# Kernel tuning notes

Hardware: AMD Instinct MI355X
Metric: run time of the kernel (lower is better)

The kernel has to match this reference:

```python
import jax, jax.numpy as jnp
import numpy as np

N = 32768   # total nodes
B = 128     # graphs
S = 256     # nodes per graph (equal-size graphs)
E = 524288  # edges
DIN = 128   # in_dim
DH = 256    # hidden_dim
H = 8       # heads
DFF = 1024  # ffn hidden
EPS = 1e-5


def _seg_sum(x, idx, num):
    return jax.ops.segment_sum(x, idx, num_segments=num)


def _bn(x, g, b):
    # BatchNorm1d with batch statistics (training-mode math, deterministic)
    mu = jnp.mean(x, axis=0)
    var = jnp.mean((x - mu) ** 2, axis=0)
    return (x - mu) * jax.lax.rsqrt(var + EPS) * g + b


def _ln(x, g, b):
    mu = jnp.mean(x, axis=-1, keepdims=True)
    var = jnp.mean((x - mu) ** 2, axis=-1, keepdims=True)
    return (x - mu) * jax.lax.rsqrt(var + EPS) * g + b


def _gcn_conv(x, W, bias, edge_index, n):
    # PyG GCNConv: h = x W; add self-loops; norm = d^-1/2[row] * d^-1/2[col]; scatter-add at col
    h = x @ W
    loop = jnp.arange(n)
    row = jnp.concatenate([edge_index[0], loop])
    col = jnp.concatenate([edge_index[1], loop])
    deg = _seg_sum(jnp.ones_like(col, dtype=h.dtype), col, n)  # >=1 due to self-loops
    dis = jax.lax.rsqrt(jnp.maximum(deg, 1.0))
    norm = dis[row] * dis[col]
    out = _seg_sum(h[row] * norm[:, None], col, n)
    return out + bias


def setup_inputs() -> dict:
    key = jax.random.key(0)
    ks = jax.random.split(key, 24)

    def w(i, shape, scale=0.05):
        return jax.random.normal(ks[i], shape, dtype=jnp.float32) * scale

    return {
        "x": jax.random.normal(ks[0], (N, DIN), dtype=jnp.float32),
        "edge_index": jax.random.randint(ks[1], (2, E), 0, N, dtype=jnp.int32),
        "batch": jnp.repeat(jnp.arange(B, dtype=jnp.int32), S),
        "inter_f": jax.random.normal(ks[2], (B, DH), dtype=jnp.float32),
        "bn1_g": jnp.ones((DIN,), jnp.float32), "bn1_b": jnp.zeros((DIN,), jnp.float32),
        "bn2_g": jnp.ones((DH,), jnp.float32), "bn2_b": jnp.zeros((DH,), jnp.float32),
        "w_conv1": w(3, (DIN, DH)), "b_conv1": jnp.zeros((DH,), jnp.float32),
        "w_conv2": w(4, (DH, DH)), "b_conv2": jnp.zeros((DH,), jnp.float32),
        "wq": w(5, (DH, DH)), "bq": jnp.zeros((DH,), jnp.float32),
        "wk": w(6, (DH, DH)), "bk": jnp.zeros((DH,), jnp.float32),
        "wv": w(7, (DH, DH)), "bv": jnp.zeros((DH,), jnp.float32),
        "wo": w(8, (DH, DH)), "bo": jnp.zeros((DH,), jnp.float32),
        "ln1_g": jnp.ones((DH,), jnp.float32), "ln1_b": jnp.zeros((DH,), jnp.float32),
        "ln2_g": jnp.ones((DH,), jnp.float32), "ln2_b": jnp.zeros((DH,), jnp.float32),
        "w_ff1": w(9, (DH, DFF)), "b_ff1": jnp.zeros((DFF,), jnp.float32),
        "w_ff2": w(10, (DFF, DH)), "b_ff2": jnp.zeros((DH,), jnp.float32),
    }


def reference(x, edge_index, batch, inter_f,
              bn1_g, bn1_b, bn2_g, bn2_b,
              w_conv1, b_conv1, w_conv2, b_conv2,
              wq, bq, wk, bk, wv, bv, wo, bo,
              ln1_g, ln1_b, ln2_g, ln2_b,
              w_ff1, b_ff1, w_ff2, b_ff2):
    n = x.shape[0]
    hd = DH // H
    # init_avg_h: scatter-mean of raw x per graph
    cnt = _seg_sum(jnp.ones((n,), x.dtype), batch, B)
    init_avg_h = _seg_sum(x, batch, B) / jnp.maximum(cnt, 1.0)[:, None]
    # layer 1 (dropout = identity in eval)
    h = _bn(x, bn1_g, bn1_b)
    h = jax.nn.relu(_gcn_conv(h, w_conv1, b_conv1, edge_index, n))
    # layer 2 with residual
    pre = h
    h2 = _bn(h, bn2_g, bn2_b)
    h = pre + jax.nn.relu(_gcn_conv(h2, w_conv2, b_conv2, edge_index, n))
    # transformer block: inject per-graph feature, self-attend within each graph
    inter_h = inter_f[batch]
    t = (h + inter_h).reshape(B, S, DH)
    q = (t @ wq + bq).reshape(B, S, H, hd)
    k = (t @ wk + bk).reshape(B, S, H, hd)
    v = (t @ wv + bv).reshape(B, S, H, hd)
    scores = jnp.einsum('bqhd,bkhd->bhqk', q, k) / jnp.sqrt(jnp.float32(hd))
    attn = jax.nn.softmax(scores, axis=-1)
    o = jnp.einsum('bhqk,bkhd->bqhd', attn, v).reshape(B, S, DH) @ wo + bo
    t2 = _ln(t + o, ln1_g, ln1_b)
    ffn = jax.nn.relu(t2 @ w_ff1 + b_ff1) @ w_ff2 + b_ff2
    t3 = _ln(t2 + ffn, ln2_g, ln2_b)
    hg = t3.reshape(n, DH)
    readout = _seg_sum(hg, batch, B)
    return readout, init_avg_h
```

## Files before the change

kernel.cpp:

```cpp
#include <hip/hip_runtime.h>
#include <math.h>

#define NN   32768
#define BG   128
#define SG   256
#define EE   524288
#define DIN_ 128
#define DH_  256
#define NH   8
#define HD_  32
#define DFF_ 1024
#define EPS_ 1e-5f

typedef __attribute__((ext_vector_type(8))) short bf16x8;
typedef __attribute__((ext_vector_type(4))) float f32x4;
typedef __attribute__((ext_vector_type(2))) unsigned int u32x2;
typedef __attribute__((ext_vector_type(4))) unsigned int u32x4;

__device__ __forceinline__ unsigned short f2bf(float f) {
    unsigned int u = __builtin_bit_cast(unsigned int, f);
    unsigned int r = u + 0x7FFFu + ((u >> 16) & 1u);
    return (unsigned short)(r >> 16);
}
__device__ __forceinline__ float bf2f(unsigned short u) {
    return __builtin_bit_cast(float, (unsigned int)u << 16);
}
__device__ __forceinline__ void glds16(const unsigned short* g, unsigned short* l) {
    __builtin_amdgcn_global_load_lds(
        (const __attribute__((address_space(1))) void*)g,
        (__attribute__((address_space(3))) void*)l, 16, 0, 0);
}
#define WAIT_VM0() __builtin_amdgcn_s_waitcnt(0x0F70)
#define WAIT_VM1() __builtin_amdgcn_s_waitcnt(0x0F71)
#define WAIT_VM2() __builtin_amdgcn_s_waitcnt(0x0F72)
#define WAIT_VM3() __builtin_amdgcn_s_waitcnt(0x0F73)
#define WAIT_VM4() __builtin_amdgcn_s_waitcnt(0x0F74)

#define QSCALE (0.17677669529663689f * 1.4426950408889634f)

__global__ __launch_bounds__(128) void initstats_kernel(const float* __restrict__ X,
                                                        float* __restrict__ out2,
                                                        float* __restrict__ csum,
                                                        float* __restrict__ csumsq) {
    int b = blockIdx.x, j = threadIdx.x;
    float s = 0.f, sq = 0.f;
    for (int r = 0; r < SG; ++r) {
        float v = X[(size_t)(b * SG + r) * DIN_ + j];
        s += v; sq += v * v;
    }
    out2[b * DIN_ + j] = s * (1.f / (float)SG);
    atomicAdd(&csum[j], s);
    atomicAdd(&csumsq[j], sq);
}

template <int C>
__global__ __launch_bounds__(C) void bnfin_kernel(const float* __restrict__ csum,
                                                  const float* __restrict__ csumsq,
                                                  const float* __restrict__ g,
                                                  const float* __restrict__ b,
                                                  float* __restrict__ scale,
                                                  float* __restrict__ shift) {
    int j = threadIdx.x;
    float mu  = csum[j] * (1.f / (float)NN);
    float var = csumsq[j] * (1.f / (float)NN) - mu * mu;
    float s = g[j] * rsqrtf(var + EPS_);
    scale[j] = s;
    shift[j] = b[j] - mu * s;
}

template <int C>
__global__ __launch_bounds__(256) void bnapply_kernel(const float* __restrict__ X,
                                                      const float* __restrict__ sc,
                                                      const float* __restrict__ sh,
                                                      unsigned short* __restrict__ Y) {
    int i = blockIdx.x * 256 + threadIdx.x;
    int j = i & (C - 1);
    Y[i] = f2bf(X[i] * sc[j] + sh[j]);
}

__global__ __launch_bounds__(256) void wtrans_kernel(const float* __restrict__ W,
                                                     unsigned short* __restrict__ Wt,
                                                     int K, int N, float scale) {
    int idx = blockIdx.x * 256 + threadIdx.x;
    if (idx < K * N) {
        int n = idx / K, k = idx - n * K;
        Wt[idx] = f2bf(W[(size_t)k * N + n] * scale);
    }
}

__global__ __launch_bounds__(256) void bcat_kernel(const float* __restrict__ bq,
                                                   const float* __restrict__ bk,
                                                   const float* __restrict__ bv,
                                                   float* __restrict__ o) {
    int j = threadIdx.x;
    if (blockIdx.x == 0) o[j] = bq[j] * QSCALE;
    else if (blockIdx.x == 1) o[DH_ + j] = bk[j];
    else o[2 * DH_ + j] = bv[j];
}

__global__ __launch_bounds__(256) void deg_kernel(const int* __restrict__ col,
                                                  int* __restrict__ deg) {
    int e = blockIdx.x * 256 + threadIdx.x;
    if (e < EE) atomicAdd(&deg[col[e]], 1);
}

__global__ __launch_bounds__(1024) void scan_kernel(const int* __restrict__ deg,
                                                    int* __restrict__ off,
                                                    float* __restrict__ dis) {
    __shared__ int sums[1024];
    int t = threadIdx.x;
    int base = t * 32;
    int loc[32];
    int run = 0;
#pragma unroll
    for (int i = 0; i < 32; ++i) { loc[i] = run; run += deg[base + i]; }
    sums[t] = run;
    __syncthreads();
    for (int d = 1; d < 1024; d <<= 1) {
        int tmp = (t >= d) ? sums[t - d] : 0;
        __syncthreads();
        sums[t] += tmp;
        __syncthreads();
    }
    int excl = sums[t] - run;
#pragma unroll
    for (int i = 0; i < 32; ++i) {
        off[base + i] = excl + loc[i];
        dis[base + i] = rsqrtf((float)(deg[base + i] + 1));
    }
    if (t == 1023) off[NN] = sums[1023];
}

__global__ __launch_bounds__(256) void scatter_kernel(const int* __restrict__ row,
                                                      const int* __restrict__ col,
                                                      const int* __restrict__ off,
                                                      int* __restrict__ cnt,
                                                      int* __restrict__ srow) {
    int e = blockIdx.x * 256 + threadIdx.x;
    if (e < EE) {
        int c = col[e];
        int p = off[c] + atomicAdd(&cnt[c], 1);
        srow[p] = row[e];
    }
}

template <int C, int FUSE_BN>
__global__ __launch_bounds__(256) void aggb_kernel(const unsigned short* __restrict__ X,
                                                   const int* __restrict__ off,
                                                   const int* __restrict__ srow,
                                                   const float* __restrict__ dis,
                                                   const float* __restrict__ scl,
                                                   const float* __restrict__ shf,
                                                   unsigned short* __restrict__ Y) {
    constexpr int EPL = C / 64;
    int lane = threadIdx.x & 63;
    int c = blockIdx.x * 4 + (threadIdx.x >> 6);
    float dc = dis[c];
    float acc[EPL];
    float wsum = dc;
    {
        unsigned short t[EPL];
        const unsigned short* xc = X + (size_t)c * C + lane * EPL;
        if constexpr (EPL == 4) *(uint2*)t = *(const uint2*)xc;
        else *(unsigned int*)t = *(const unsigned int*)xc;
#pragma unroll
        for (int e2 = 0; e2 < EPL; ++e2) acc[e2] = dc * bf2f(t[e2]);
    }
    int s = off[c], en = off[c + 1];
    int i = s;
    for (; i + 4 <= en; i += 4) {
        int r0 = srow[i], r1 = srow[i + 1], r2 = srow[i + 2], r3 = srow[i + 3];
        float d0 = dis[r0], d1 = dis[r1], d2 = dis[r2], d3 = dis[r3];
        unsigned short t0[EPL], t1[EPL], t2[EPL], t3[EPL];
        const unsigned short* p0 = X + (size_t)r0 * C + lane * EPL;
        const unsigned short* p1 = X + (size_t)r1 * C + lane * EPL;
        const unsigned short* p2 = X + (size_t)r2 * C + lane * EPL;
        const unsigned short* p3 = X + (size_t)r3 * C + lane * EPL;
        if constexpr (EPL == 4) {
            *(uint2*)t0 = *(const uint2*)p0;
            *(uint2*)t1 = *(const uint2*)p1;
            *(uint2*)t2 = *(const uint2*)p2;
            *(uint2*)t3 = *(const uint2*)p3;
        } else {
            *(unsigned int*)t0 = *(const unsigned int*)p0;
            *(unsigned int*)t1 = *(const unsigned int*)p1;
            *(unsigned int*)t2 = *(const unsigned int*)p2;
            *(unsigned int*)t3 = *(const unsigned int*)p3;
        }
        wsum += d0 + d1 + d2 + d3;
#pragma unroll
        for (int e2 = 0; e2 < EPL; ++e2) {
            acc[e2] += d0 * bf2f(t0[e2]) + d1 * bf2f(t1[e2]) +
                       d2 * bf2f(t2[e2]) + d3 * bf2f(t3[e2]);
        }
    }
    for (; i < en; ++i) {
        int r = srow[i];
        float dr = dis[r];
        unsigned short t[EPL];
        const unsigned short* xr = X + (size_t)r * C + lane * EPL;
        if constexpr (EPL == 4) *(uint2*)t = *(const uint2*)xr;
        else *(unsigned int*)t = *(const unsigned int*)xr;
        wsum += dr;
#pragma unroll
        for (int e2 = 0; e2 < EPL; ++e2) acc[e2] += dr * bf2f(t[e2]);
    }
    unsigned short t[EPL];
#pragma unroll
    for (int e2 = 0; e2 < EPL; ++e2) {
        float v;
        if constexpr (FUSE_BN) {
            int j = lane * EPL + e2;
            v = dc * (scl[j] * acc[e2] + shf[j] * wsum);
        } else {
            v = dc * acc[e2];
        }
        t[e2] = f2bf(v);
    }
    unsigned short* yc = Y + (size_t)c * C + lane * EPL;
    if constexpr (EPL == 4) *(uint2*)yc = *(const uint2*)t;
    else *(unsigned int*)yc = *(const unsigned int*)t;
}

__global__ __launch_bounds__(512, 8) void gemm_bf16_kernel(
    const unsigned short* __restrict__ A,
    const unsigned short* __restrict__ Bt,
    unsigned short* __restrict__ Cb,
    int M, int K, int N,
    const float* __restrict__ bias,
    const unsigned short* __restrict__ resb,
    const float* __restrict__ inter,
    int do_relu, int relu_first) {
    constexpr int LDP = 32;
    constexpr int CP = 136;
    constexpr int MI = 2;
    constexpr int STG = 8192;
    constexpr int BOFS = 4096;
    __shared__ unsigned short Smem[3 * STG];
    unsigned short* Cs = Smem;
    int gx = gridDim.x, gyP = gridDim.y >> 3;
    int d = blockIdx.y * gx + blockIdx.x;
    int xcd = d & 7, j2 = d >> 3;
    int bm = (xcd * gyP + j2 / gx) * 128;
    int bn = (j2 % gx) * 128;
    int tid = threadIdx.x;
    int wave = tid >> 6, lane = tid & 63;
    int wm = (wave >> 1) * 32;
    int wn = (wave & 1) * 64;
    int lrc = lane & 15;
    int koct = lane >> 4;
    int rsw = (lrc >> 1) & 3;
    int rofs = (koct ^ rsw) * 8;
    int cg = (lane & 3) ^ ((lane >> 3) & 3);
    int skk = cg * 8;

    int sr = wave * 16 + (lane >> 2);
    const unsigned short* gA0 = A + (size_t)(bm + sr) * K + skk;
    const unsigned short* gB0 = Bt + (size_t)(bn + sr) * K + skk;
    int lofs = wave * 512 + lane * 8;

    f32x4 acc[MI][4];
#pragma unroll
    for (int i = 0; i < MI; ++i)
#pragma unroll
        for (int j = 0; j < 4; ++j) acc[i][j] = (f32x4){0.f, 0.f, 0.f, 0.f};

    glds16(gA0, Smem + lofs);
    glds16(gB0, Smem + BOFS + lofs);
    glds16(gA0 + 32, Smem + STG + lofs);
    glds16(gB0 + 32, Smem + STG + BOFS + lofs);

    int rb = 0;
    for (int k0 = 0; k0 < K; k0 += 32) {
        if (k0 + 64 < K) {
            int wb = rb + 2; if (wb >= 3) wb -= 3;
            unsigned short* ld = Smem + wb * STG;
            glds16(gA0 + k0 + 64, ld + lofs);
            glds16(gB0 + k0 + 64, ld + BOFS + lofs);
            WAIT_VM4();
        } else if (k0 + 32 < K) {
            WAIT_VM2();
        } else {
            WAIT_VM0();
        }
        __builtin_amdgcn_s_barrier();
        const unsigned short* Ab = Smem + rb * STG;
        const unsigned short* Bb = Ab + BOFS;
        bf16x8 af[MI], bfr[4];
#pragma unroll
        for (int i = 0; i < MI; ++i)
            af[i] = *(const bf16x8*)(Ab + (wm + i * 16 + lrc) * LDP + rofs);
#pragma unroll
        for (int j = 0; j < 4; ++j)
            bfr[j] = *(const bf16x8*)(Bb + (wn + j * 16 + lrc) * LDP + rofs);
#pragma unroll
        for (int i = 0; i < MI; ++i)
#pragma unroll
            for (int j = 0; j < 4; ++j)
                acc[i][j] = __builtin_amdgcn_mfma_f32_16x16x32_bf16(af[i], bfr[j],
                                                                    acc[i][j], 0, 0, 0);
        __builtin_amdgcn_s_barrier();
        rb = (rb + 1 == 3) ? 0 : rb + 1;
    }
#pragma unroll
    for (int i = 0; i < MI; ++i) {
#pragma unroll
        for (int r = 0; r < 4; ++r) {
            int lrow = wm + i * 16 + koct * 4 + r;
            int grow = bm + lrow;
#pragma unroll
            for (int j = 0; j < 4; ++j) {
                int lcol = wn + j * 16 + lrc;
                int gcol = bn + lcol;
                float v = acc[i][j][r];
                if (bias) v += bias[gcol];
                if (relu_first) v = fmaxf(v, 0.f);
                if (resb) v += bf2f(resb[(size_t)grow * N + gcol]);
                if (inter) v += inter[(grow >> 8) * N + gcol];
                if (do_relu && !relu_first) v = fmaxf(v, 0.f);
                Cs[lrow * CP + lcol] = f2bf(v);
            }
        }
    }
    __syncthreads();
#pragma unroll
    for (int it = 0; it < 4; ++it) {
        int row = it * 32 + (tid >> 4);
        int cc = (tid & 15) * 8;
        *(uint4*)(&Cb[(size_t)(bm + row) * N + bn + cc]) =
            *(const uint4*)(&Cs[row * CP + cc]);
    }
}

template <int MODE>
__global__ __launch_bounds__(512, 8) void gemm32n256_kernel(
    const unsigned short* __restrict__ A,
    const unsigned short* __restrict__ Bt,
    unsigned short* __restrict__ Cb,
    int K,
    const float* __restrict__ bias,
    const unsigned short* __restrict__ resb,
    const float* __restrict__ inter,
    int do_relu, int relu_first,
    float* __restrict__ stat0, float* __restrict__ stat1,
    const float* __restrict__ lng, const float* __restrict__ lnbt,
    float* __restrict__ outp) {
    constexpr int LDP = 32;
    constexpr int CP = 264;
    constexpr int STG = 9216;
    constexpr int BOFS = 1024;
    __shared__ unsigned short Smem[2 * STG];
    unsigned short* Cs = Smem;
    int bm = blockIdx.x * 32;
    int tid = threadIdx.x;
    int wave = tid >> 6, lane = tid & 63;
    int wm = (wave >> 2) * 16;
    int wn = (wave & 3) * 64;
    int lrc = lane & 15;
    int koct = lane >> 4;
    int rsw = (lrc >> 1) & 3;
    int rofs = (koct ^ rsw) * 8;
    int cg = (lane & 3) ^ ((lane >> 3) & 3);
    int skk = cg * 8;

    const unsigned short* gB0 = Bt + (size_t)(wave * 32 + (lane >> 2)) * K + skk;
    size_t g16 = (size_t)16 * K;
    int lofsB = BOFS + wave * 1024 + lane * 8;
    const unsigned short* gA0 = nullptr;
    int lofsA = 0;
    if (wave < 2) {
        gA0 = A + (size_t)(bm + wave * 16 + (lane >> 2)) * K + skk;
        lofsA = wave * 512 + lane * 8;
    }

    f32x4 acc[4];
#pragma unroll
    for (int j = 0; j < 4; ++j) acc[j] = (f32x4){0.f, 0.f, 0.f, 0.f};

    glds16(gB0, Smem + lofsB);
    glds16(gB0 + g16, Smem + lofsB + 512);
    if (wave < 2) glds16(gA0, Smem + lofsA);

    int cur = 0;
    for (int k0 = 0; k0 < K; k0 += 32) {
        int nk = k0 + 32;
        if (nk < K) {
            unsigned short* nb = Smem + (cur ^ 1) * STG;
            glds16(gB0 + nk, nb + lofsB);
            glds16(gB0 + nk + g16, nb + lofsB + 512);
            if (wave < 2) {
                glds16(gA0 + nk, nb + lofsA);
                WAIT_VM3();
            } else {
                WAIT_VM2();
            }
        } else {
            WAIT_VM0();
        }
        __builtin_amdgcn_s_barrier();
        const unsigned short* Ab = Smem + cur * STG;
        const unsigned short* Bb = Ab + BOFS;
        bf16x8 af = *(const bf16x8*)(Ab + (wm + lrc) * LDP + rofs);
        bf16x8 bfr[4];
#pragma unroll
        for (int j = 0; j < 4; ++j)
            bfr[j] = *(const bf16x8*)(Bb + (wn + j * 16 + lrc) * LDP + rofs);
#pragma unroll
        for (int j = 0; j < 4; ++j)
            acc[j] = __builtin_amdgcn_mfma_f32_16x16x32_bf16(af, bfr[j], acc[j], 0, 0, 0);
        __builtin_amdgcn_s_barrier();
        cur ^= 1;
    }
#pragma unroll
    for (int r = 0; r < 4; ++r) {
        int lrow = wm + koct * 4 + r;
        int grow = bm + lrow;
#pragma unroll
        for (int j = 0; j < 4; ++j) {
            int lcol = wn + j * 16 + lrc;
            float v = acc[j][r];
            if (bias) v += bias[lcol];
            if (relu_first) v = fmaxf(v, 0.f);
            if (resb) v += bf2f(resb[(size_t)grow * 256 + lcol]);
            if (inter) v += inter[(grow >> 8) * 256 + lcol];
            if (do_relu && !relu_first) v = fmaxf(v, 0.f);
            Cs[lrow * CP + lcol] = f2bf(v);
        }
    }
    __syncthreads();

    if constexpr (MODE == 0 || MODE == 1) {
#pragma unroll
        for (int it = 0; it < 2; ++it) {
            int row = it * 16 + (tid >> 5);
            int cc = (tid & 31) * 8;
            *(uint4*)(&Cb[(size_t)(bm + row) * 256 + cc]) =
                *(const uint4*)(&Cs[row * CP + cc]);
        }
        if constexpr (MODE == 1) {
            if (tid < 256) {
                float s = 0.f, sq = 0.f;
                for (int r = 0; r < 32; ++r) {
                    float v = bf2f(Cs[r * CP + tid]);
                    s += v; sq += v * v;
                }
                atomicAdd(&stat0[tid], s);
                atomicAdd(&stat1[tid], sq);
            }
        }
    } else {
        float4 g4 = *(const float4*)(lng + lane * 4);
        float4 b4 = *(const float4*)(lnbt + lane * 4);
#pragma unroll
        for (int q = 0; q < 4; ++q) {
            int row = wave * 4 + q;
            unsigned short tv[4];
            *(uint2*)tv = *(const uint2*)(Cs + row * CP + lane * 4);
            float v0 = bf2f(tv[0]), v1 = bf2f(tv[1]), v2 = bf2f(tv[2]), v3 = bf2f(tv[3]);
            float sum = v0 + v1 + v2 + v3;
#pragma unroll
            for (int off = 32; off; off >>= 1) sum += __shfl_xor(sum, off);
            float mu = sum * (1.f / (float)DH_);
            float d0 = v0 - mu, d1 = v1 - mu, d2 = v2 - mu, d3 = v3 - mu;
            float vs = d0 * d0 + d1 * d1 + d2 * d2 + d3 * d3;
#pragma unroll
            for (int off = 32; off; off >>= 1) vs += __shfl_xor(vs, off);
            float rs = rsqrtf(vs * (1.f / (float)DH_) + EPS_);
            unsigned short ov[4];
            ov[0] = f2bf(d0 * rs * g4.x + b4.x);
            ov[1] = f2bf(d1 * rs * g4.y + b4.y);
            ov[2] = f2bf(d2 * rs * g4.z + b4.z);
            ov[3] = f2bf(d3 * rs * g4.w + b4.w);
            if constexpr (MODE == 2) {
                *(uint2*)(&Cb[(size_t)(bm + row) * 256 + lane * 4]) = *(uint2*)ov;
            } else {
                *(uint2*)(Cs + row * CP + lane * 4) = *(uint2*)ov;
            }
        }
        if constexpr (MODE == 3) {
            __syncthreads();
            if (tid < 256) {
                float s = 0.f;
                for (int r = 0; r < 32; ++r) s += bf2f(Cs[r * CP + tid]);
                atomicAdd(&outp[(bm >> 8) * 256 + tid], s);
            }
        }
    }
}

__global__ __launch_bounds__(256, 4) void attn_mfma_kernel(
    const unsigned short* __restrict__ QKV,
    unsigned short* __restrict__ Ob) {
    int b = blockIdx.x >> 3, h = blockIdx.x & 7;
    __shared__ unsigned short Ks[256 * 32];
    __shared__ unsigned short Vt[32 * 264];
    __shared__ float Lc[4 * 64];
    const unsigned short* kg = QKV + (size_t)b * 256 * 768 + 256 + h * 32;
    const unsigned short* vg = QKV + (size_t)b * 256 * 768 + 512 + h * 32;
    int tid = threadIdx.x;
#pragma unroll
    for (int it = 0; it < 4; ++it) {
        int c = it * 256 + tid;
        int row = c >> 2, ch = c & 3;
        int slot = ch ^ ((row >> 1) & 3);
        *(uint4*)(Ks + row * 32 + slot * 8) =
            *(const uint4*)(kg + (size_t)row * 768 + ch * 8);
    }
#pragma unroll
    for (int it = 0; it < 4; ++it) {
        int c = it * 256 + tid;
        int key = c >> 2, d0 = (c & 3) * 8;
        unsigned short tmp[8];
        *(uint4*)tmp = *(const uint4*)(vg + (size_t)key * 768 + d0);
#pragma unroll
        for (int j = 0; j < 8; ++j) Vt[(d0 + j) * 264 + key] = tmp[j];
    }
    __syncthreads();

    int wave = tid >> 6, lane = tid & 63;
    int lr = lane & 15, koct = lane >> 4;
    int s4 = (lr >> 1) & 3;
    int qrow0 = b * 256 + wave * 64;
    bf16x8 qf[4];
#pragma unroll
    for (int j = 0; j < 4; ++j)
        qf[j] = *(const bf16x8*)(QKV + (size_t)(qrow0 + j * 16 + lr) * 768 + h * 32 + koct * 8);

    f32x4 Oa[4][2];
    float lp[4];
#pragma unroll
    for (int i = 0; i < 4; ++i) {
        Oa[i][0] = (f32x4){0.f, 0.f, 0.f, 0.f};
        Oa[i][1] = (f32x4){0.f, 0.f, 0.f, 0.f};
        lp[i] = 0.f;
    }
    float* Lw = Lc + wave * 64;

    for (int kc = 0; kc < 256; kc += 32) {
        bf16x8 kf0 = *(const bf16x8*)(Ks + (kc + lr) * 32 + (koct ^ s4) * 8);
        bf16x8 kf1 = *(const bf16x8*)(Ks + (kc + 16 + lr) * 32 + (koct ^ s4) * 8);
        bf16x8 pfr[4];
#pragma unroll
        for (int j = 0; j < 4; ++j) {
            f32x4 St0 = __builtin_amdgcn_mfma_f32_16x16x32_bf16(kf0, qf[j],
                            (f32x4){0.f, 0.f, 0.f, 0.f}, 0, 0, 0);
            f32x4 St1 = __builtin_amdgcn_mfma_f32_16x16x32_bf16(kf1, qf[j],
                            (f32x4){0.f, 0.f, 0.f, 0.f}, 0, 0, 0);
            float p0[4], p1[4], ps = 0.f;
#pragma unroll
            for (int r = 0; r < 4; ++r) {
                p0[r] = exp2f(St0[r]); p1[r] = exp2f(St1[r]);
                ps += p0[r] + p1[r];
            }
            lp[j] += ps;
            unsigned int w0a, w0b, w1a, w1b;
            asm("v_cvt_pk_bf16_f32 %0, %1, %2" : "=v"(w0a) : "v"(p0[0]), "v"(p0[1]));
            asm("v_cvt_pk_bf16_f32 %0, %1, %2" : "=v"(w0b) : "v"(p0[2]), "v"(p0[3]));
            asm("v_cvt_pk_bf16_f32 %0, %1, %2" : "=v"(w1a) : "v"(p1[0]), "v"(p1[1]));
            asm("v_cvt_pk_bf16_f32 %0, %1, %2" : "=v"(w1b) : "v"(p1[2]), "v"(p1[3]));
            u32x2 sa = __builtin_amdgcn_permlane32_swap(w0a, w1a, false, false);
            u32x2 da = __builtin_amdgcn_permlane16_swap(sa[0], sa[1], false, false);
            u32x2 sb = __builtin_amdgcn_permlane32_swap(w0b, w1b, false, false);
            u32x2 db = __builtin_amdgcn_permlane16_swap(sb[0], sb[1], false, false);
            u32x4 pw = {da[0], db[0], da[1], db[1]};
            pfr[j] = __builtin_bit_cast(bf16x8, pw);
        }
        bf16x8 vf0 = *(const bf16x8*)(Vt + lr * 264 + kc + koct * 8);
        bf16x8 vf1 = *(const bf16x8*)(Vt + (16 + lr) * 264 + kc + koct * 8);
#pragma unroll
        for (int i = 0; i < 4; ++i) {
            Oa[i][0] = __builtin_amdgcn_mfma_f32_16x16x32_bf16(pfr[i], vf0, Oa[i][0], 0, 0, 0);
            Oa[i][1] = __builtin_amdgcn_mfma_f32_16x16x32_bf16(pfr[i], vf1, Oa[i][1], 0, 0, 0);
        }
    }
#pragma unroll
    for (int j = 0; j < 4; ++j) {
        lp[j] += __shfl_xor(lp[j], 16);
        lp[j] += __shfl_xor(lp[j], 32);
    }
    if (koct == 0) {
#pragma unroll
        for (int j = 0; j < 4; ++j) Lw[j * 16 + lr] = lp[j];
    }
    __builtin_amdgcn_s_waitcnt(0);
#pragma unroll
    for (int i = 0; i < 4; ++i) {
        f32x4 l4 = *(const f32x4*)(Lw + i * 16 + koct * 4);
#pragma unroll
        for (int r = 0; r < 4; ++r) {
            float inv = 1.f / l4[r];
            int row = qrow0 + i * 16 + koct * 4 + r;
#pragma unroll
            for (int jn = 0; jn < 2; ++jn) {
                int col = h * 32 + jn * 16 + lr;
                Ob[(size_t)row * 256 + col] = f2bf(Oa[i][jn][r] * inv);
            }
        }
    }
}

extern "C" void kernel_launch(void* const* d_in, const int* in_sizes, int n_in,
                              void* d_out, int out_size, void* d_ws, size_t ws_size,
                              hipStream_t stream) {
    const float* x       = (const float*)d_in[0];
    const int*   ei      = (const int*)d_in[1];
    const float* inter_f = (const float*)d_in[3];
    const float* bn1_g = (const float*)d_in[4],  *bn1_b = (const float*)d_in[5];
    const float* bn2_g = (const float*)d_in[6],  *bn2_b = (const float*)d_in[7];
    const float* w_conv1 = (const float*)d_in[8],  *b_conv1 = (const float*)d_in[9];
    const float* w_conv2 = (const float*)d_in[10], *b_conv2 = (const float*)d_in[11];
    const float* wq = (const float*)d_in[12], *bq = (const float*)d_in[13];
    const float* wk = (const float*)d_in[14], *bk = (const float*)d_in[15];
    const float* wv = (const float*)d_in[16], *bv = (const float*)d_in[17];
    const float* wo = (const float*)d_in[18], *bo = (const float*)d_in[19];
    const float* ln1_g = (const float*)d_in[20], *ln1_b = (const float*)d_in[21];
    const float* ln2_g = (const float*)d_in[22], *ln2_b = (const float*)d_in[23];
    const float* w_ff1 = (const float*)d_in[24], *b_ff1 = (const float*)d_in[25];
    const float* w_ff2 = (const float*)d_in[26], *b_ff2 = (const float*)d_in[27];
    float* out = (float*)d_out;

    char* base = (char*)d_ws;
    size_t o = 0;
    auto alloc = [&](size_t bytes) -> void* {
        void* p = base + o;
        o = (o + bytes + 255) & ~(size_t)255;
        return p;
    };
    int*   deg    = (int*)alloc(NN * 4);
    int*   off    = (int*)alloc((NN + 1) * 4);
    int*   cnt    = (int*)alloc(NN * 4);
    int*   srow   = (int*)alloc(EE * 4);
    float* dis    = (float*)alloc(NN * 4);
    float* csum   = (float*)alloc(256 * 4);
    float* csumsq = (float*)alloc(256 * 4);
    float* csum2  = (float*)alloc(256 * 4);
    float* csumsq2= (float*)alloc(256 * 4);
    float* scl    = (float*)alloc(256 * 4);
    float* shf    = (float*)alloc(256 * 4);
    float* bqkv   = (float*)alloc(768 * 4);
    const size_t SLOT = (size_t)NN * DH_;
    unsigned short* Arena = (unsigned short*)alloc((size_t)NN * DFF_ * 2);
    unsigned short* TB = (unsigned short*)alloc(SLOT * 2);
    unsigned short* B0 = (unsigned short*)alloc(SLOT * 2);
    unsigned short* wc1t  = (unsigned short*)alloc((size_t)DIN_ * DH_ * 2);
    unsigned short* wc2t  = (unsigned short*)alloc((size_t)DH_ * DH_ * 2);
    unsigned short* wqkvt = (unsigned short*)alloc((size_t)DH_ * DH_ * 3 * 2);
    unsigned short* wot   = (unsigned short*)alloc((size_t)DH_ * DH_ * 2);
    unsigned short* wf1t  = (unsigned short*)alloc((size_t)DH_ * DFF_ * 2);
    unsigned short* wf2t  = (unsigned short*)alloc((size_t)DFF_ * DH_ * 2);
    unsigned short* Xa   = Arena;
    unsigned short* X2a  = Arena + (size_t)NN * DIN_;
    unsigned short* QKVb = Arena;
    unsigned short* Fb   = Arena;
    unsigned short* tb   = TB;

    hipMemsetAsync(deg, 0, NN * 4, stream);
    hipMemsetAsync(cnt, 0, NN * 4, stream);
    hipMemsetAsync(csum, 0, 4096, stream);
    hipMemsetAsync(out, 0, BG * DH_ * 4, stream);

    wtrans_kernel<<<(DIN_ * DH_ + 255) / 256, 256, 0, stream>>>(w_conv1, wc1t, DIN_, DH_, 1.f);
    wtrans_kernel<<<(DH_ * DH_ + 255) / 256, 256, 0, stream>>>(w_conv2, wc2t, DH_, DH_, 1.f);
    wtrans_kernel<<<(DH_ * DH_ + 255) / 256, 256, 0, stream>>>(wq, wqkvt, DH_, DH_, QSCALE);
    wtrans_kernel<<<(DH_ * DH_ + 255) / 256, 256, 0, stream>>>(wk, wqkvt + DH_ * DH_, DH_, DH_, 1.f);
    wtrans_kernel<<<(DH_ * DH_ + 255) / 256, 256, 0, stream>>>(wv, wqkvt + 2 * DH_ * DH_, DH_, DH_, 1.f);
    wtrans_kernel<<<(DH_ * DH_ + 255) / 256, 256, 0, stream>>>(wo, wot, DH_, DH_, 1.f);
    wtrans_kernel<<<(DH_ * DFF_ + 255) / 256, 256, 0, stream>>>(w_ff1, wf1t, DH_, DFF_, 1.f);
    wtrans_kernel<<<(DFF_ * DH_ + 255) / 256, 256, 0, stream>>>(w_ff2, wf2t, DFF_, DH_, 1.f);
    bcat_kernel<<<3, 256, 0, stream>>>(bq, bk, bv, bqkv);

    initstats_kernel<<<BG, 128, 0, stream>>>(x, out + BG * DH_, csum, csumsq);
    bnfin_kernel<DIN_><<<1, DIN_, 0, stream>>>(csum, csumsq, bn1_g, bn1_b, scl, shf);
    bnapply_kernel<DIN_><<<NN * DIN_ / 256, 256, 0, stream>>>(x, scl, shf, B0);

    deg_kernel<<<EE / 256, 256, 0, stream>>>(ei + EE, deg);
    scan_kernel<<<1, 1024, 0, stream>>>(deg, off, dis);
    scatter_kernel<<<EE / 256, 256, 0, stream>>>(ei, ei + EE, off, cnt, srow);

    aggb_kernel<DIN_, 0><<<NN / 4, 256, 0, stream>>>(B0, off, srow, dis,
                                                     nullptr, nullptr, Xa);
    gemm32n256_kernel<1><<<NN / 32, 512, 0, stream>>>(
        Xa, wc1t, B0, DIN_, b_conv1, nullptr, nullptr, 1, 0,
        csum2, csumsq2, nullptr, nullptr, nullptr);
    bnfin_kernel<DH_><<<1, DH_, 0, stream>>>(csum2, csumsq2, bn2_g, bn2_b, scl, shf);

    aggb_kernel<DH_, 1><<<NN / 4, 256, 0, stream>>>(B0, off, srow, dis,
                                                    scl, shf, X2a);
    gemm32n256_kernel<0><<<NN / 32, 512, 0, stream>>>(
        X2a, wc2t, tb, DH_, b_conv2, B0, inter_f, 1, 1,
        nullptr, nullptr, nullptr, nullptr, nullptr);

    gemm_bf16_kernel<<<dim3(768 / 128, NN / 128), 512, 0, stream>>>(
        tb, wqkvt, QKVb, NN, DH_, 768, bqkv, nullptr, nullptr, 0, 0);

    attn_mfma_kernel<<<BG * NH, 256, 0, stream>>>(QKVb, B0);

    gemm32n256_kernel<2><<<NN / 32, 512, 0, stream>>>(
        B0, wot, B0, DH_, bo, tb, nullptr, 0, 0,
        nullptr, nullptr, ln1_g, ln1_b, nullptr);

    gemm_bf16_kernel<<<dim3(DFF_ / 128, NN / 128), 512, 0, stream>>>(
        B0, wf1t, Fb, NN, DH_, DFF_, b_ff1, nullptr, nullptr, 1, 0);

    gemm32n256_kernel<3><<<NN / 32, 512, 0, stream>>>(
        Fb, wf2t, nullptr, DFF_, b_ff2, B0, nullptr, 0, 0,
        nullptr, nullptr, ln2_g, ln2_b, out);
}
```

Baseline: 533.1 us.

## Widen row-tile GEMM to 64 rows with triple-buffered async LDS loads

Doubles the M tile of the N=256 GEMM from 32 to 64 rows, so each wave computes two 16-row MFMA fragments and reuses its B fragments across them. It also moves from double to triple buffering, prefetching two k-steps ahead with adjusted vmcnt waits. This halves the number of times B tiles are re-read per row and gives more latency hiding. In exchange it halves the block count and raises LDS and register use, which lowers occupancy.

```diff
diff --git a/kernel.cpp b/kernel.cpp
--- a/kernel.cpp
+++ b/kernel.cpp
@@ -35,6 +35,7 @@
 #define WAIT_VM2() __builtin_amdgcn_s_waitcnt(0x0F72)
 #define WAIT_VM3() __builtin_amdgcn_s_waitcnt(0x0F73)
 #define WAIT_VM4() __builtin_amdgcn_s_waitcnt(0x0F74)
+#define WAIT_VM6() __builtin_amdgcn_s_waitcnt(0x0F76)
 
 #define QSCALE (0.17677669529663689f * 1.4426950408889634f)
 
@@ -333,7 +334,7 @@
 }
 
 template <int MODE>
-__global__ __launch_bounds__(512, 8) void gemm32n256_kernel(
+__global__ __launch_bounds__(512, 4) void gemm64n256_kernel(
     const unsigned short* __restrict__ A,
     const unsigned short* __restrict__ Bt,
     unsigned short* __restrict__ Cb,
@@ -347,14 +348,14 @@
     float* __restrict__ outp) {
     constexpr int LDP = 32;
     constexpr int CP = 264;
-    constexpr int STG = 9216;
-    constexpr int BOFS = 1024;
-    __shared__ unsigned short Smem[2 * STG];
+    constexpr int STG = 10240;
+    constexpr int BOFS = 2048;
+    __shared__ unsigned short Smem[3 * STG];
     unsigned short* Cs = Smem;
-    int bm = blockIdx.x * 32;
+    int bm = blockIdx.x * 64;
     int tid = threadIdx.x;
     int wave = tid >> 6, lane = tid & 63;
-    int wm = (wave >> 2) * 16;
+    int wm = (wave >> 2) * 32;
     int wn = (wave & 3) * 64;
     int lrc = lane & 15;
     int koct = lane >> 4;
@@ -368,70 +369,86 @@
     int lofsB = BOFS + wave * 1024 + lane * 8;
     const unsigned short* gA0 = nullptr;
     int lofsA = 0;
-    if (wave < 2) {
+    if (wave < 4) {
         gA0 = A + (size_t)(bm + wave * 16 + (lane >> 2)) * K + skk;
         lofsA = wave * 512 + lane * 8;
     }
 
-    f32x4 acc[4];
-#pragma unroll
-    for (int j = 0; j < 4; ++j) acc[j] = (f32x4){0.f, 0.f, 0.f, 0.f};
-
-    glds16(gB0, Smem + lofsB);
-    glds16(gB0 + g16, Smem + lofsB + 512);
-    if (wave < 2) glds16(gA0, Smem + lofsA);
-
-    int cur = 0;
+    f32x4 acc[2][4];
+#pragma unroll
+    for (int i = 0; i < 2; ++i)
+#pragma unroll
+        for (int j = 0; j < 4; ++j) acc[i][j] = (f32x4){0.f, 0.f, 0.f, 0.f};
+
+#pragma unroll
+    for (int st = 0; st < 2; ++st) {
+        unsigned short* s = Smem + st * STG;
+        glds16(gB0 + st * 32, s + lofsB);
+        glds16(gB0 + st * 32 + g16, s + lofsB + 512);
+        if (wave < 4) glds16(gA0 + st * 32, s + lofsA);
+    }
+
+    int rb = 0;
     for (int k0 = 0; k0 < K; k0 += 32) {
-        int nk = k0 + 32;
-        if (nk < K) {
-            unsigned short* nb = Smem + (cur ^ 1) * STG;
-            glds16(gB0 + nk, nb + lofsB);
-            glds16(gB0 + nk + g16, nb + lofsB + 512);
-            if (wave < 2) {
-                glds16(gA0 + nk, nb + lofsA);
-                WAIT_VM3();
+        if (k0 + 64 < K) {
+            int wb = rb + 2; if (wb >= 3) wb -= 3;
+            unsigned short* s = Smem + wb * STG;
+            glds16(gB0 + k0 + 64, s + lofsB);
+            glds16(gB0 + k0 + 64 + g16, s + lofsB + 512);
+            if (wave < 4) {
+                glds16(gA0 + k0 + 64, s + lofsA);
+                WAIT_VM6();
             } else {
-                WAIT_VM2();
+                WAIT_VM4();
             }
+        } else if (k0 + 32 < K) {
+            if (wave < 4) WAIT_VM3(); else WAIT_VM2();
         } else {
             WAIT_VM0();
         }
         __builtin_amdgcn_s_barrier();
-        const unsigned short* Ab = Smem + cur * STG;
+        const unsigned short* Ab = Smem + rb * STG;
         const unsigned short* Bb = Ab + BOFS;
-        bf16x8 af = *(const bf16x8*)(Ab + (wm + lrc) * LDP + rofs);
-        bf16x8 bfr[4];
+        bf16x8 af[2], bfr[4];
+#pragma unroll
+        for (int i = 0; i < 2; ++i)
+            af[i] = *(const bf16x8*)(Ab + (wm + i * 16 + lrc) * LDP + rofs);
 #pragma unroll
         for (int j = 0; j < 4; ++j)
             bfr[j] = *(const bf16x8*)(Bb + (wn + j * 16 + lrc) * LDP + rofs);
 #pragma unroll
-        for (int j = 0; j < 4; ++j)
-            acc[j] = __builtin_amdgcn_mfma_f32_16x16x32_bf16(af, bfr[j], acc[j], 0, 0, 0);
+        for (int i = 0; i < 2; ++i)
+#pragma unroll
+            for (int j = 0; j < 4; ++j)
+                acc[i][j] = __builtin_amdgcn_mfma_f32_16x16x32_bf16(af[i], bfr[j],
+                                                                    acc[i][j], 0, 0, 0);
         __builtin_amdgcn_s_barrier();
-        cur ^= 1;
-    }
-#pragma unroll
-    for (int r = 0; r < 4; ++r) {
-        int lrow = wm + koct * 4 + r;
-        int grow = bm + lrow;
-#pragma unroll
-        for (int j = 0; j < 4; ++j) {
-            int lcol = wn + j * 16 + lrc;
-            float v = acc[j][r];
-            if (bias) v += bias[lcol];
-            if (relu_first) v = fmaxf(v, 0.f);
-            if (resb) v += bf2f(resb[(size_t)grow * 256 + lcol]);
-            if (inter) v += inter[(grow >> 8) * 256 + lcol];
-            if (do_relu && !relu_first) v = fmaxf(v, 0.f);
-            Cs[lrow * CP + lcol] = f2bf(v);
+        rb = (rb + 1 == 3) ? 0 : rb + 1;
+    }
+#pragma unroll
+    for (int i = 0; i < 2; ++i) {
+#pragma unroll
+        for (int r = 0; r < 4; ++r) {
+            int lrow = wm + i * 16 + koct * 4 + r;
+            int grow = bm + lrow;
+#pragma unroll
+            for (int j = 0; j < 4; ++j) {
+                int lcol = wn + j * 16 + lrc;
+                float v = acc[i][j][r];
+                if (bias) v += bias[lcol];
+                if (relu_first) v = fmaxf(v, 0.f);
+                if (resb) v += bf2f(resb[(size_t)grow * 256 + lcol]);
+                if (inter) v += inter[(grow >> 8) * 256 + lcol];
+                if (do_relu && !relu_first) v = fmaxf(v, 0.f);
+                Cs[lrow * CP + lcol] = f2bf(v);
+            }
         }
     }
     __syncthreads();
 
     if constexpr (MODE == 0 || MODE == 1) {
 #pragma unroll
-        for (int it = 0; it < 2; ++it) {
+        for (int it = 0; it < 4; ++it) {
             int row = it * 16 + (tid >> 5);
             int cc = (tid & 31) * 8;
             *(uint4*)(&Cb[(size_t)(bm + row) * 256 + cc]) =
@@ -440,7 +457,7 @@
         if constexpr (MODE == 1) {
             if (tid < 256) {
                 float s = 0.f, sq = 0.f;
-                for (int r = 0; r < 32; ++r) {
+                for (int r = 0; r < 64; ++r) {
                     float v = bf2f(Cs[r * CP + tid]);
                     s += v; sq += v * v;
                 }
@@ -452,8 +469,8 @@
         float4 g4 = *(const float4*)(lng + lane * 4);
         float4 b4 = *(const float4*)(lnbt + lane * 4);
 #pragma unroll
-        for (int q = 0; q < 4; ++q) {
-            int row = wave * 4 + q;
+        for (int q = 0; q < 8; ++q) {
+            int row = wave * 8 + q;
             unsigned short tv[4];
             *(uint2*)tv = *(const uint2*)(Cs + row * CP + lane * 4);
             float v0 = bf2f(tv[0]), v1 = bf2f(tv[1]), v2 = bf2f(tv[2]), v3 = bf2f(tv[3]);
@@ -481,7 +498,7 @@
             __syncthreads();
             if (tid < 256) {
                 float s = 0.f;
-                for (int r = 0; r < 32; ++r) s += bf2f(Cs[r * CP + tid]);
+                for (int r = 0; r < 64; ++r) s += bf2f(Cs[r * CP + tid]);
                 atomicAdd(&outp[(bm >> 8) * 256 + tid], s);
             }
         }
@@ -679,14 +696,14 @@
 
     aggb_kernel<DIN_, 0><<<NN / 4, 256, 0, stream>>>(B0, off, srow, dis,
                                                      nullptr, nullptr, Xa);
-    gemm32n256_kernel<1><<<NN / 32, 512, 0, stream>>>(
+    gemm64n256_kernel<1><<<NN / 64, 512, 0, stream>>>(
         Xa, wc1t, B0, DIN_, b_conv1, nullptr, nullptr, 1, 0,
         csum2, csumsq2, nullptr, nullptr, nullptr);
     bnfin_kernel<DH_><<<1, DH_, 0, stream>>>(csum2, csumsq2, bn2_g, bn2_b, scl, shf);
 
     aggb_kernel<DH_, 1><<<NN / 4, 256, 0, stream>>>(B0, off, srow, dis,
                                                     scl, shf, X2a);
-    gemm32n256_kernel<0><<<NN / 32, 512, 0, stream>>>(
+    gemm64n256_kernel<0><<<NN / 64, 512, 0, stream>>>(
         X2a, wc2t, tb, DH_, b_conv2, B0, inter_f, 1, 1,
         nullptr, nullptr, nullptr, nullptr, nullptr);
 
@@ -695,14 +712,14 @@
 
     attn_mfma_kernel<<<BG * NH, 256, 0, stream>>>(QKVb, B0);
 
-    gemm32n256_kernel<2><<<NN / 32, 512, 0, stream>>>(
+    gemm64n256_kernel<2><<<NN / 64, 512, 0, stream>>>(
         B0, wot, B0, DH_, bo, tb, nullptr, 0, 0,
         nullptr, nullptr, ln1_g, ln1_b, nullptr);
 
     gemm_bf16_kernel<<<dim3(DFF_ / 128, NN / 128), 512, 0, stream>>>(
         B0, wf1t, Fb, NN, DH_, DFF_, b_ff1, nullptr, nullptr, 1, 0);
 
-    gemm32n256_kernel<3><<<NN / 32, 512, 0, stream>>>(
+    gemm64n256_kernel<3><<<NN / 64, 512, 0, stream>>>(
         Fb, wf2t, nullptr, DFF_, b_ff2, B0, nullptr, 0, 0,
         nullptr, nullptr, ln2_g, ln2_b, out);
 }
```

Measured after the change: 521.7 us. 1.02x faster.
